# Performance work log

Measured on AMD Instinct MI355X. Metric: run time of the kernel, lower is better.

## Reference

```python
import jax, jax.numpy as jnp
import numpy as np

N_NODES = 100000
N_EDGES = 1600000
D_FEAT = 64


def setup_inputs() -> dict:
    key = jax.random.key(0)
    k1, k2, k3 = jax.random.split(key, 3)
    features = jax.random.normal(k1, (N_NODES, D_FEAT), dtype=jnp.float32)
    row = jax.random.randint(k2, (N_EDGES,), 0, N_NODES, dtype=jnp.int64 if jax.config.jax_enable_x64 else jnp.int32)
    col = jax.random.randint(k3, (N_EDGES,), 0, N_NODES, dtype=jnp.int64 if jax.config.jax_enable_x64 else jnp.int32)
    return {"features": features, "row": row, "col": col}


def reference(features, row, col):
    # adj @ H  ==  segment-sum of H[col] grouped by row (COO SpMM)
    n = features.shape[0]
    gathered = features[col]                                  # [E, d] irregular gather
    summed = jax.ops.segment_sum(gathered, row, num_segments=n)  # [N, d]
    # deg = clip(adj.sum(1), 1, None) -> per-row nonzero count
    ones = jnp.ones((row.shape[0],), dtype=features.dtype)
    deg = jax.ops.segment_sum(ones, row, num_segments=n)
    deg = jnp.clip(deg, 1.0, None)
    agg = summed / deg[:, None]
    # combine: residual add
    return features + agg
```

## Files before the change

### kernel.cpp

```cpp
#include <hip/hip_runtime.h>

#define D_FEAT 64
#define CB 256
#define CBITS 8
#define NB2MAX 512
#define E_BLK 8192
#define TMAX 256
#define SCAP 4608

__device__ inline unsigned short f2bf(float f) {
    unsigned u = __float_as_uint(f);
    u += 0x7FFFu + ((u >> 16) & 1u);
    return (unsigned short)(u >> 16);
}
__device__ inline float bf_lo(unsigned u) { return __uint_as_float(u << 16); }
__device__ inline float bf_hi(unsigned u) { return __uint_as_float(u & 0xFFFF0000u); }

__global__ __launch_bounds__(1024, 4)
void bin5_conv_kernel(const int* __restrict__ row, const int* __restrict__ col,
                      int* __restrict__ tilebuf,
                      int* __restrict__ csumG,
                      int n_edges, int ebt, int nb2,
                      const float* __restrict__ feat,
                      unsigned short* __restrict__ feat_bf, int n4) {
    int gb = blockIdx.x;
    int t = threadIdx.x;
    if (gb < ebt) {
        __shared__ int hist[NB2MAX];
        __shared__ int scn[NB2MAX];
        __shared__ int ebuf[E_BLK];
        for (int i = t; i < nb2; i += 1024) hist[i] = 0;
        __syncthreads();
        int e0 = gb * E_BLK, e1 = min(e0 + E_BLK, n_edges);
        int ne = e1 - e0;
        int rr[8], cc[8];
        #pragma unroll
        for (int k = 0; k < 8; ++k) {
            int i = t + k * 1024;
            if (i < ne) { rr[k] = row[e0 + i]; cc[k] = col[e0 + i]; }
            else rr[k] = -1;
        }
        #pragma unroll
        for (int k = 0; k < 8; ++k)
            if (rr[k] >= 0) atomicAdd(&hist[rr[k] >> CBITS], 1);
        __syncthreads();
        if (t < nb2) scn[t] = hist[t];
        __syncthreads();
        for (int o = 1; o < nb2; o <<= 1) {
            int v = (t < nb2 && t >= o) ? scn[t - o] : 0;
            __syncthreads();
            if (t < nb2) scn[t] += v;
            __syncthreads();
        }
        if (t < nb2) hist[t] = scn[t] - hist[t];
        __syncthreads();
        for (int i = t; i < nb2 + 1; i += 1024)
            csumG[(size_t)gb * (nb2 + 1) + i] = (i < nb2) ? hist[i] : ne;
        __syncthreads();
        #pragma unroll
        for (int k = 0; k < 8; ++k) {
            if (rr[k] >= 0) {
                int b = rr[k] >> CBITS;
                int pos = atomicAdd(&hist[b], 1);
                ebuf[pos] = ((rr[k] & (CB - 1)) << 17) | cc[k];
            }
        }
        __syncthreads();
        for (int i = t; i < ne; i += 1024)
            tilebuf[(size_t)gb * E_BLK + i] = ebuf[i];
    } else {
        int i = (gb - ebt) * 1024 + t;
        if (i < n4) {
            float4 f = reinterpret_cast<const float4*>(feat)[i];
            ushort4 u;
            u.x = f2bf(f.x); u.y = f2bf(f.y); u.z = f2bf(f.z); u.w = f2bf(f.w);
            reinterpret_cast<ushort4*>(feat_bf)[i] = u;
        }
    }
}

template<int BF>
__global__ __launch_bounds__(1024, 8)
void agg7_kernel(const float* __restrict__ feat,
                 const unsigned short* __restrict__ feat_bf,
                 const int* __restrict__ tilebuf,
                 const int* __restrict__ csumG,
                 float* __restrict__ out, int n_nodes, int ebt, int nb2) {
    __shared__ int tstart[TMAX], tlen[TMAX], psum[TMAX];
    __shared__ int scol[SCAP];
    __shared__ int cnt[CB], csum[CB], cur[CB], ddeg[CB];

    int cb = blockIdx.x;
    int t = threadIdx.x;
    int w = t >> 6, lane = t & 63;
    int q = lane >> 3, sub = lane & 7;
    int rA = w * 16 + q;
    int rB = rA + 8;

    for (int i = t; i < ebt; i += 1024) {
        int s = csumG[(size_t)i * (nb2 + 1) + cb];
        int e = csumG[(size_t)i * (nb2 + 1) + cb + 1];
        tstart[i] = s; tlen[i] = e - s;
    }
    if (t < CB) ddeg[t] = 0;
    __syncthreads();
    if (t < ebt) psum[t] = tlen[t];
    __syncthreads();
    for (int o = 1; o < ebt; o <<= 1) {
        int v = (t < ebt && t >= o) ? psum[t - o] : 0;
        __syncthreads();
        if (t < ebt) psum[t] += v;
        __syncthreads();
    }
    int total = psum[ebt - 1];

    float acc[16];
    #pragma unroll
    for (int k = 0; k < 16; ++k) acc[k] = 0.f;

#define GATHER(cv, o0)                                                         \
    do {                                                                       \
        if (BF) {                                                              \
            uint4 d = *reinterpret_cast<const uint4*>(                         \
                feat_bf + (size_t)(cv)*D_FEAT + sub * 8);                      \
            acc[o0+0] += bf_lo(d.x); acc[o0+1] += bf_hi(d.x);                  \
            acc[o0+2] += bf_lo(d.y); acc[o0+3] += bf_hi(d.y);                  \
            acc[o0+4] += bf_lo(d.z); acc[o0+5] += bf_hi(d.z);                  \
            acc[o0+6] += bf_lo(d.w); acc[o0+7] += bf_hi(d.w);                  \
        } else {                                                               \
            float4 x0 = *reinterpret_cast<const float4*>(                      \
                feat + (size_t)(cv)*D_FEAT + sub * 8);                         \
            float4 x1 = *reinterpret_cast<const float4*>(                      \
                feat + (size_t)(cv)*D_FEAT + sub * 8 + 4);                     \
            acc[o0+0] += x0.x; acc[o0+1] += x0.y;                              \
            acc[o0+2] += x0.z; acc[o0+3] += x0.w;                              \
            acc[o0+4] += x1.x; acc[o0+5] += x1.y;                              \
            acc[o0+6] += x1.z; acc[o0+7] += x1.w;                              \
        }                                                                      \
    } while (0)

    for (int L = 0; L < total; L += SCAP) {
        int R = min(L + SCAP, total);
        if (t < CB) cnt[t] = 0;
        __syncthreads();
        for (int tt = w; tt < ebt; tt += 16) {
            int pre = psum[tt] - tlen[tt];
            int lo = max(L - pre, 0), hi = min(tlen[tt], R - pre);
            const int* tp = tilebuf + (size_t)tt * E_BLK + tstart[tt];
            for (int i = lo + lane; i < hi; i += 64)
                atomicAdd(&cnt[((unsigned)tp[i]) >> 17], 1);
        }
        __syncthreads();
        if (t < CB) csum[t] = cnt[t];
        __syncthreads();
        for (int o = 1; o < CB; o <<= 1) {
            int v = (t < CB && t >= o) ? csum[t - o] : 0;
            __syncthreads();
            if (t < CB) csum[t] += v;
            __syncthreads();
        }
        if (t < CB) { cur[t] = csum[t] - cnt[t]; ddeg[t] += cnt[t]; }
        __syncthreads();
        for (int tt = w; tt < ebt; tt += 16) {
            int pre = psum[tt] - tlen[tt];
            int lo = max(L - pre, 0), hi = min(tlen[tt], R - pre);
            const int* tp = tilebuf + (size_t)tt * E_BLK + tstart[tt];
            for (int i = lo + lane; i < hi; i += 64) {
                int pk = tp[i];
                scol[atomicAdd(&cur[((unsigned)pk) >> 17], 1)] = pk & 0x1FFFF;
            }
        }
        __syncthreads();
        int cA = cnt[rA], sA = csum[rA] - cA;
        int cB2 = cnt[rB], sB = csum[rB] - cB2;
        int m = max(cA, cB2);
        #pragma unroll 2
        for (int j = 0; j < m; ++j) {
            if (j < cA) { int c = scol[sA + j]; GATHER(c, 0); }
            if (j < cB2) { int c = scol[sB + j]; GATHER(c, 8); }
        }
        __syncthreads();
    }
#undef GATHER

    {
        int r = cb * CB + rA;
        if (r < n_nodes) {
            float inv = 1.0f / fmaxf((float)ddeg[rA], 1.0f);
            size_t off = (size_t)r * D_FEAT + sub * 8;
            float4 f0 = *reinterpret_cast<const float4*>(feat + off);
            float4 f1 = *reinterpret_cast<const float4*>(feat + off + 4);
            float4 o0, o1;
            o0.x = f0.x + acc[0] * inv; o0.y = f0.y + acc[1] * inv;
            o0.z = f0.z + acc[2] * inv; o0.w = f0.w + acc[3] * inv;
            o1.x = f1.x + acc[4] * inv; o1.y = f1.y + acc[5] * inv;
            o1.z = f1.z + acc[6] * inv; o1.w = f1.w + acc[7] * inv;
            *reinterpret_cast<float4*>(out + off) = o0;
            *reinterpret_cast<float4*>(out + off + 4) = o1;
        }
        r = cb * CB + rB;
        if (r < n_nodes) {
            float inv = 1.0f / fmaxf((float)ddeg[rB], 1.0f);
            size_t off = (size_t)r * D_FEAT + sub * 8;
            float4 f0 = *reinterpret_cast<const float4*>(feat + off);
            float4 f1 = *reinterpret_cast<const float4*>(feat + off + 4);
            float4 o0, o1;
            o0.x = f0.x + acc[8]  * inv; o0.y = f0.y + acc[9]  * inv;
            o0.z = f0.z + acc[10] * inv; o0.w = f0.w + acc[11] * inv;
            o1.x = f1.x + acc[12] * inv; o1.y = f1.y + acc[13] * inv;
            o1.z = f1.z + acc[14] * inv; o1.w = f1.w + acc[15] * inv;
            *reinterpret_cast<float4*>(out + off) = o0;
            *reinterpret_cast<float4*>(out + off + 4) = o1;
        }
    }
}

extern "C" void kernel_launch(void* const* d_in, const int* in_sizes, int n_in,
                              void* d_out, int out_size, void* d_ws, size_t ws_size,
                              hipStream_t stream) {
    const float* feat = (const float*)d_in[0];
    const int* row = (const int*)d_in[1];
    const int* col = (const int*)d_in[2];
    float* out = (float*)d_out;

    const int n_nodes = in_sizes[0] / D_FEAT;
    const int n_edges = in_sizes[1];
    const int nb2 = (n_nodes + CB - 1) / CB;
    const int ebt = (n_edges + E_BLK - 1) / E_BLK;
    const int n4 = n_nodes * D_FEAT / 4;

    size_t tb_bytes  = (size_t)ebt * E_BLK * 4;
    size_t cs_bytes  = (size_t)ebt * (nb2 + 1) * 4;
    size_t bf_bytes  = (size_t)n_nodes * D_FEAT * 2;

    size_t lean_need = tb_bytes + cs_bytes + 256;
    size_t fat_need  = lean_need + ((bf_bytes + 63) & ~(size_t)63);
    bool fat = (ws_size >= fat_need);

    char* ws = (char*)d_ws;
    size_t p = 0;
    int* tilebuf = (int*)(ws + p); p += tb_bytes;
    int* csumG   = (int*)(ws + p); p += cs_bytes;
    p = (p + 63) & ~(size_t)63;
    unsigned short* feat_bf = nullptr;
    if (fat) { feat_bf = (unsigned short*)(ws + p); }

    {
        int conv_blocks = fat ? (n4 + 1023) / 1024 : 0;
        bin5_conv_kernel<<<ebt + conv_blocks, 1024, 0, stream>>>(
            row, col, tilebuf, csumG, n_edges, ebt, nb2,
            feat, feat_bf, fat ? n4 : 0);
    }
    if (fat) {
        agg7_kernel<1><<<nb2, 1024, 0, stream>>>(
            feat, feat_bf, tilebuf, csumG, out, n_nodes, ebt, nb2);
    } else {
        agg7_kernel<0><<<nb2, 1024, 0, stream>>>(
            feat, nullptr, tilebuf, csumG, out, n_nodes, ebt, nb2);
    }
}
```

Baseline: 134.7 us.

## Sub-sort edges by column slab and flatten tile traversal with binary search

The binning kernel now uses 512-thread blocks with 4096-edge tiles, and replaces its shared-memory Hillis-Steele scan with a wave-shuffle scan. The aggregation kernel loads each edge once into registers, finding its source tile by binary search over the prefix sums, instead of reading the tile buffer twice per chunk. It then counting-sorts edges by (row, column slab) so gathers within a slab touch a narrower range of feature rows, aiming for better L2 locality. The cost is more shared memory (bigger key arrays and a 1024-wide scan), lower occupancy (launch bounds 2 instead of 8), and eight slab passes per chunk, each ending in a barrier.

```diff
diff --git a/kernel.cpp b/kernel.cpp
--- a/kernel.cpp
+++ b/kernel.cpp
@@ -3,10 +3,14 @@
 #define D_FEAT 64
 #define CB 256
 #define CBITS 8
-#define NB2MAX 512
-#define E_BLK 8192
-#define TMAX 256
+#define NBC 448
+#define NSLAB 8
+#define SLBITS 14
+#define E_BLK 4096
+#define TMAX 512
 #define SCAP 4608
+#define KEYS (CB * NSLAB)
+#define PKN 5
 
 __device__ inline unsigned short f2bf(float f) {
     unsigned u = __float_as_uint(f);
@@ -16,8 +20,8 @@
 __device__ inline float bf_lo(unsigned u) { return __uint_as_float(u << 16); }
 __device__ inline float bf_hi(unsigned u) { return __uint_as_float(u & 0xFFFF0000u); }
 
-__global__ __launch_bounds__(1024, 4)
-void bin5_conv_kernel(const int* __restrict__ row, const int* __restrict__ col,
+__global__ __launch_bounds__(512, 4)
+void bin6_conv_kernel(const int* __restrict__ row, const int* __restrict__ col,
                       int* __restrict__ tilebuf,
                       int* __restrict__ csumG,
                       int n_edges, int ebt, int nb2,
@@ -26,17 +30,18 @@
     int gb = blockIdx.x;
     int t = threadIdx.x;
     if (gb < ebt) {
-        __shared__ int hist[NB2MAX];
-        __shared__ int scn[NB2MAX];
+        __shared__ int hist[NBC];
         __shared__ int ebuf[E_BLK];
-        for (int i = t; i < nb2; i += 1024) hist[i] = 0;
+        __shared__ int wpart[8];
+        int w = t >> 6, lane = t & 63;
+        for (int i = t; i < nb2; i += 512) hist[i] = 0;
         __syncthreads();
         int e0 = gb * E_BLK, e1 = min(e0 + E_BLK, n_edges);
         int ne = e1 - e0;
         int rr[8], cc[8];
         #pragma unroll
         for (int k = 0; k < 8; ++k) {
-            int i = t + k * 1024;
+            int i = t + k * 512;
             if (i < ne) { rr[k] = row[e0 + i]; cc[k] = col[e0 + i]; }
             else rr[k] = -1;
         }
@@ -44,18 +49,31 @@
         for (int k = 0; k < 8; ++k)
             if (rr[k] >= 0) atomicAdd(&hist[rr[k] >> CBITS], 1);
         __syncthreads();
-        if (t < nb2) scn[t] = hist[t];
-        __syncthreads();
-        for (int o = 1; o < nb2; o <<= 1) {
-            int v = (t < nb2 && t >= o) ? scn[t - o] : 0;
-            __syncthreads();
-            if (t < nb2) scn[t] += v;
-            __syncthreads();
-        }
-        if (t < nb2) hist[t] = scn[t] - hist[t];
-        __syncthreads();
-        for (int i = t; i < nb2 + 1; i += 1024)
-            csumG[(size_t)gb * (nb2 + 1) + i] = (i < nb2) ? hist[i] : ne;
+        int idx = w * 64 + lane;
+        int v = 0, incl = 0;
+        if (w < 7) {
+            v = (idx < nb2) ? hist[idx] : 0;
+            incl = v;
+            #pragma unroll
+            for (int o = 1; o < 64; o <<= 1) {
+                int up = __shfl_up(incl, o, 64);
+                if (lane >= o) incl += up;
+            }
+            if (lane == 63) wpart[w] = incl;
+        }
+        __syncthreads();
+        if (t == 0) {
+            int run = 0;
+            #pragma unroll
+            for (int k = 0; k < 7; ++k) { int x = wpart[k]; wpart[k] = run; run += x; }
+        }
+        __syncthreads();
+        if (w < 7 && idx < nb2) {
+            int excl = incl - v + wpart[w];
+            csumG[(size_t)gb * (nb2 + 1) + idx] = excl;
+            hist[idx] = excl;
+        }
+        if (t == 0) csumG[(size_t)gb * (nb2 + 1) + nb2] = ne;
         __syncthreads();
         #pragma unroll
         for (int k = 0; k < 8; ++k) {
@@ -66,10 +84,10 @@
             }
         }
         __syncthreads();
-        for (int i = t; i < ne; i += 1024)
+        for (int i = t; i < ne; i += 512)
             tilebuf[(size_t)gb * E_BLK + i] = ebuf[i];
     } else {
-        int i = (gb - ebt) * 1024 + t;
+        int i = (gb - ebt) * 512 + t;
         if (i < n4) {
             float4 f = reinterpret_cast<const float4*>(feat)[i];
             ushort4 u;
@@ -80,15 +98,18 @@
 }
 
 template<int BF>
-__global__ __launch_bounds__(1024, 8)
-void agg7_kernel(const float* __restrict__ feat,
+__global__ __launch_bounds__(1024, 2)
+void agg8_kernel(const float* __restrict__ feat,
                  const unsigned short* __restrict__ feat_bf,
                  const int* __restrict__ tilebuf,
                  const int* __restrict__ csumG,
                  float* __restrict__ out, int n_nodes, int ebt, int nb2) {
     __shared__ int tstart[TMAX], tlen[TMAX], psum[TMAX];
     __shared__ int scol[SCAP];
-    __shared__ int cnt[CB], csum[CB], cur[CB], ddeg[CB];
+    __shared__ int cnt2[KEYS], incl2[KEYS], cur2[KEYS];
+    __shared__ int ddeg[CB];
+    __shared__ int sred[1024];
+    __shared__ int wpart[8];
 
     int cb = blockIdx.x;
     int t = threadIdx.x;
@@ -104,12 +125,27 @@
     }
     if (t < CB) ddeg[t] = 0;
     __syncthreads();
-    if (t < ebt) psum[t] = tlen[t];
-    __syncthreads();
-    for (int o = 1; o < ebt; o <<= 1) {
-        int v = (t < ebt && t >= o) ? psum[t - o] : 0;
-        __syncthreads();
-        if (t < ebt) psum[t] += v;
+    {
+        int idx = w * 64 + lane;
+        int v = 0, incl = 0;
+        if (w < 7) {
+            v = (idx < ebt) ? tlen[idx] : 0;
+            incl = v;
+            #pragma unroll
+            for (int o = 1; o < 64; o <<= 1) {
+                int up = __shfl_up(incl, o, 64);
+                if (lane >= o) incl += up;
+            }
+            if (lane == 63) wpart[w] = incl;
+        }
+        __syncthreads();
+        if (t == 0) {
+            int run = 0;
+            #pragma unroll
+            for (int k = 0; k < 7; ++k) { int x = wpart[k]; wpart[k] = run; run += x; }
+        }
+        __syncthreads();
+        if (w < 7 && idx < ebt) psum[idx] = incl + wpart[w];
         __syncthreads();
     }
     int total = psum[ebt - 1];
@@ -141,45 +177,69 @@
 
     for (int L = 0; L < total; L += SCAP) {
         int R = min(L + SCAP, total);
-        if (t < CB) cnt[t] = 0;
-        __syncthreads();
-        for (int tt = w; tt < ebt; tt += 16) {
-            int pre = psum[tt] - tlen[tt];
-            int lo = max(L - pre, 0), hi = min(tlen[tt], R - pre);
-            const int* tp = tilebuf + (size_t)tt * E_BLK + tstart[tt];
-            for (int i = lo + lane; i < hi; i += 64)
-                atomicAdd(&cnt[((unsigned)tp[i]) >> 17], 1);
-        }
-        __syncthreads();
-        if (t < CB) csum[t] = cnt[t];
-        __syncthreads();
-        for (int o = 1; o < CB; o <<= 1) {
-            int v = (t < CB && t >= o) ? csum[t - o] : 0;
+        for (int i = t; i < KEYS; i += 1024) cnt2[i] = 0;
+        __syncthreads();
+        int pkr[PKN];
+        #pragma unroll
+        for (int k = 0; k < PKN; ++k) {
+            int j = L + t + k * 1024;
+            pkr[k] = -1;
+            if (j < R) {
+                int lo = 0, hi = ebt - 1;
+                #pragma unroll 9
+                while (lo < hi) { int mid = (lo + hi) >> 1;
+                                  if (psum[mid] > j) hi = mid; else lo = mid + 1; }
+                int local = j - (psum[lo] - tlen[lo]);
+                pkr[k] = tilebuf[(size_t)lo * E_BLK + tstart[lo] + local];
+            }
+        }
+        #pragma unroll
+        for (int k = 0; k < PKN; ++k) {
+            if (pkr[k] >= 0) {
+                int key = (((unsigned)pkr[k]) >> 17) * NSLAB
+                        + ((pkr[k] & 0x1FFFF) >> SLBITS);
+                atomicAdd(&cnt2[key], 1);
+            }
+        }
+        __syncthreads();
+        int a = cnt2[2 * t], bb = cnt2[2 * t + 1];
+        sred[t] = a + bb;
+        __syncthreads();
+        for (int o = 1; o < 1024; o <<= 1) {
+            int x = (t >= o) ? sred[t - o] : 0;
             __syncthreads();
-            if (t < CB) csum[t] += v;
+            sred[t] += x;
             __syncthreads();
         }
-        if (t < CB) { cur[t] = csum[t] - cnt[t]; ddeg[t] += cnt[t]; }
-        __syncthreads();
-        for (int tt = w; tt < ebt; tt += 16) {
-            int pre = psum[tt] - tlen[tt];
-            int lo = max(L - pre, 0), hi = min(tlen[tt], R - pre);
-            const int* tp = tilebuf + (size_t)tt * E_BLK + tstart[tt];
-            for (int i = lo + lane; i < hi; i += 64) {
-                int pk = tp[i];
-                scol[atomicAdd(&cur[((unsigned)pk) >> 17], 1)] = pk & 0x1FFFF;
-            }
-        }
-        __syncthreads();
-        int cA = cnt[rA], sA = csum[rA] - cA;
-        int cB2 = cnt[rB], sB = csum[rB] - cB2;
-        int m = max(cA, cB2);
-        #pragma unroll 2
-        for (int j = 0; j < m; ++j) {
-            if (j < cA) { int c = scol[sA + j]; GATHER(c, 0); }
-            if (j < cB2) { int c = scol[sB + j]; GATHER(c, 8); }
-        }
-        __syncthreads();
+        int ep = sred[t] - (a + bb);
+        incl2[2 * t] = ep + a;
+        incl2[2 * t + 1] = ep + a + bb;
+        cur2[2 * t] = ep;
+        cur2[2 * t + 1] = ep + a;
+        __syncthreads();
+        if (t < CB) ddeg[t] += incl2[t * NSLAB + NSLAB - 1]
+                             - incl2[t * NSLAB] + cnt2[t * NSLAB];
+        #pragma unroll
+        for (int k = 0; k < PKN; ++k) {
+            if (pkr[k] >= 0) {
+                int cval = pkr[k] & 0x1FFFF;
+                int key = (((unsigned)pkr[k]) >> 17) * NSLAB + (cval >> SLBITS);
+                scol[atomicAdd(&cur2[key], 1)] = cval;
+            }
+        }
+        __syncthreads();
+        for (int s = 0; s < NSLAB; ++s) {
+            int kA = rA * NSLAB + s, kB = rB * NSLAB + s;
+            int lenA = cnt2[kA], sA = incl2[kA] - lenA;
+            int lenB = cnt2[kB], sB = incl2[kB] - lenB;
+            int m = max(lenA, lenB);
+            #pragma unroll 2
+            for (int j = 0; j < m; ++j) {
+                if (j < lenA) { int c = scol[sA + j]; GATHER(c, 0); }
+                if (j < lenB) { int c = scol[sB + j]; GATHER(c, 8); }
+            }
+            __syncthreads();
+        }
     }
 #undef GATHER
 
@@ -246,16 +306,16 @@
     if (fat) { feat_bf = (unsigned short*)(ws + p); }
 
     {
-        int conv_blocks = fat ? (n4 + 1023) / 1024 : 0;
-        bin5_conv_kernel<<<ebt + conv_blocks, 1024, 0, stream>>>(
+        int conv_blocks = fat ? (n4 + 511) / 512 : 0;
+        bin6_conv_kernel<<<ebt + conv_blocks, 512, 0, stream>>>(
             row, col, tilebuf, csumG, n_edges, ebt, nb2,
             feat, feat_bf, fat ? n4 : 0);
     }
     if (fat) {
-        agg7_kernel<1><<<nb2, 1024, 0, stream>>>(
+        agg8_kernel<1><<<nb2, 1024, 0, stream>>>(
             feat, feat_bf, tilebuf, csumG, out, n_nodes, ebt, nb2);
     } else {
-        agg7_kernel<0><<<nb2, 1024, 0, stream>>>(
+        agg8_kernel<0><<<nb2, 1024, 0, stream>>>(
             feat, nullptr, tilebuf, csumG, out, n_nodes, ebt, nb2);
     }
 }
```

Result: slower. 188.8 us (+40.2%).

## Shrink row-chunks and edge tiles, load packed edges once per pass via binary search

Applied to the files above, without the earlier changes.

Halves the row-chunk size to 128 rows and the edge tile to 4096 edges, and drops blocks to 512 threads, so the aggregation grid has more, smaller blocks. In the aggregation kernel, each thread now finds its edges with a binary search over the per-tile prefix sums and keeps up to five packed edges in registers. Those edges feed both the count and the scatter phases, so tilebuf is read once per pass instead of twice. The binning kernel scans a fixed 1024-entry histogram with two elements per thread. The cost is a per-edge binary search, more partial tiles per chunk, and a larger csum table, and ebt must now fit in 512 and nb2 in 1024.

```diff
diff --git a/kernel.cpp b/kernel.cpp
--- a/kernel.cpp
+++ b/kernel.cpp
@@ -1,12 +1,13 @@
 #include <hip/hip_runtime.h>
 
 #define D_FEAT 64
-#define CB 256
-#define CBITS 8
-#define NB2MAX 512
-#define E_BLK 8192
-#define TMAX 256
-#define SCAP 4608
+#define CB 128
+#define CBITS 7
+#define NBPAD 1024
+#define E_BLK 4096
+#define EBTPAD 512
+#define SCAP 2560
+#define PKN 5
 
 __device__ inline unsigned short f2bf(float f) {
     unsigned u = __float_as_uint(f);
@@ -16,8 +17,8 @@
 __device__ inline float bf_lo(unsigned u) { return __uint_as_float(u << 16); }
 __device__ inline float bf_hi(unsigned u) { return __uint_as_float(u & 0xFFFF0000u); }
 
-__global__ __launch_bounds__(1024, 4)
-void bin5_conv_kernel(const int* __restrict__ row, const int* __restrict__ col,
+__global__ __launch_bounds__(512, 8)
+void bin7_conv_kernel(const int* __restrict__ row, const int* __restrict__ col,
                       int* __restrict__ tilebuf,
                       int* __restrict__ csumG,
                       int n_edges, int ebt, int nb2,
@@ -26,17 +27,17 @@
     int gb = blockIdx.x;
     int t = threadIdx.x;
     if (gb < ebt) {
-        __shared__ int hist[NB2MAX];
-        __shared__ int scn[NB2MAX];
+        __shared__ int hist[NBPAD];
+        __shared__ int cura[NBPAD];
         __shared__ int ebuf[E_BLK];
-        for (int i = t; i < nb2; i += 1024) hist[i] = 0;
-        __syncthreads();
-        int e0 = gb * E_BLK, e1 = min(e0 + E_BLK, n_edges);
-        int ne = e1 - e0;
+        for (int i = t; i < NBPAD; i += 512) hist[i] = 0;
+        __syncthreads();
+        int e0 = gb * E_BLK;
+        int ne = min(E_BLK, n_edges - e0);
         int rr[8], cc[8];
         #pragma unroll
         for (int k = 0; k < 8; ++k) {
-            int i = t + k * 1024;
+            int i = t + k * 512;
             if (i < ne) { rr[k] = row[e0 + i]; cc[k] = col[e0 + i]; }
             else rr[k] = -1;
         }
@@ -44,32 +45,31 @@
         for (int k = 0; k < 8; ++k)
             if (rr[k] >= 0) atomicAdd(&hist[rr[k] >> CBITS], 1);
         __syncthreads();
-        if (t < nb2) scn[t] = hist[t];
-        __syncthreads();
-        for (int o = 1; o < nb2; o <<= 1) {
-            int v = (t < nb2 && t >= o) ? scn[t - o] : 0;
-            __syncthreads();
-            if (t < nb2) scn[t] += v;
-            __syncthreads();
-        }
-        if (t < nb2) hist[t] = scn[t] - hist[t];
-        __syncthreads();
-        for (int i = t; i < nb2 + 1; i += 1024)
-            csumG[(size_t)gb * (nb2 + 1) + i] = (i < nb2) ? hist[i] : ne;
+        for (int o = 1; o < NBPAD; o <<= 1) {
+            int v0 = (t >= o) ? hist[t - o] : 0;
+            int v1 = hist[t + 512 - o];
+            __syncthreads();
+            hist[t] += v0; hist[t + 512] += v1;
+            __syncthreads();
+        }
+        cura[t] = (t == 0) ? 0 : hist[t - 1];
+        cura[t + 512] = hist[t + 511];
+        for (int i = t; i < nb2 + 1; i += 512)
+            csumG[(size_t)gb * (nb2 + 1) + i] = (i == 0) ? 0 : hist[i - 1];
         __syncthreads();
         #pragma unroll
         for (int k = 0; k < 8; ++k) {
             if (rr[k] >= 0) {
                 int b = rr[k] >> CBITS;
-                int pos = atomicAdd(&hist[b], 1);
+                int pos = atomicAdd(&cura[b], 1);
                 ebuf[pos] = ((rr[k] & (CB - 1)) << 17) | cc[k];
             }
         }
         __syncthreads();
-        for (int i = t; i < ne; i += 1024)
+        for (int i = t; i < ne; i += 512)
             tilebuf[(size_t)gb * E_BLK + i] = ebuf[i];
     } else {
-        int i = (gb - ebt) * 1024 + t;
+        int i = (gb - ebt) * 512 + t;
         if (i < n4) {
             float4 f = reinterpret_cast<const float4*>(feat)[i];
             ushort4 u;
@@ -80,36 +80,37 @@
 }
 
 template<int BF>
-__global__ __launch_bounds__(1024, 8)
-void agg7_kernel(const float* __restrict__ feat,
+__global__ __launch_bounds__(512, 8)
+void agg9_kernel(const float* __restrict__ feat,
                  const unsigned short* __restrict__ feat_bf,
                  const int* __restrict__ tilebuf,
                  const int* __restrict__ csumG,
                  float* __restrict__ out, int n_nodes, int ebt, int nb2) {
-    __shared__ int tstart[TMAX], tlen[TMAX], psum[TMAX];
+    __shared__ int tstart[EBTPAD], tlen[EBTPAD], psum[EBTPAD];
     __shared__ int scol[SCAP];
-    __shared__ int cnt[CB], csum[CB], cur[CB], ddeg[CB];
+    __shared__ int cnt[CB], incl[CB], cur[CB], ddeg[CB];
 
     int cb = blockIdx.x;
     int t = threadIdx.x;
     int w = t >> 6, lane = t & 63;
-    int q = lane >> 3, sub = lane & 7;
-    int rA = w * 16 + q;
-    int rB = rA + 8;
-
-    for (int i = t; i < ebt; i += 1024) {
+    int g = w * 8 + (lane >> 3);
+    int sub = lane & 7;
+    int rA = g;
+    int rB = g + 64;
+
+    for (int i = t; i < ebt; i += 512) {
         int s = csumG[(size_t)i * (nb2 + 1) + cb];
         int e = csumG[(size_t)i * (nb2 + 1) + cb + 1];
         tstart[i] = s; tlen[i] = e - s;
     }
     if (t < CB) ddeg[t] = 0;
     __syncthreads();
-    if (t < ebt) psum[t] = tlen[t];
+    psum[t] = (t < ebt) ? tlen[t] : 0;
     __syncthreads();
-    for (int o = 1; o < ebt; o <<= 1) {
-        int v = (t < ebt && t >= o) ? psum[t - o] : 0;
-        __syncthreads();
-        if (t < ebt) psum[t] += v;
+    for (int o = 1; o < EBTPAD; o <<= 1) {
+        int v = (t >= o) ? psum[t - o] : 0;
+        __syncthreads();
+        psum[t] += v;
         __syncthreads();
     }
     int total = psum[ebt - 1];
@@ -143,40 +144,47 @@
         int R = min(L + SCAP, total);
         if (t < CB) cnt[t] = 0;
         __syncthreads();
-        for (int tt = w; tt < ebt; tt += 16) {
-            int pre = psum[tt] - tlen[tt];
-            int lo = max(L - pre, 0), hi = min(tlen[tt], R - pre);
-            const int* tp = tilebuf + (size_t)tt * E_BLK + tstart[tt];
-            for (int i = lo + lane; i < hi; i += 64)
-                atomicAdd(&cnt[((unsigned)tp[i]) >> 17], 1);
-        }
-        __syncthreads();
-        if (t < CB) csum[t] = cnt[t];
+        int pkr[PKN];
+        #pragma unroll
+        for (int k = 0; k < PKN; ++k) {
+            int j = L + t + k * 512;
+            pkr[k] = -1;
+            if (j < R) {
+                int lo = 0, hi = ebt - 1;
+                while (lo < hi) { int mid = (lo + hi) >> 1;
+                                  if (psum[mid] > j) hi = mid; else lo = mid + 1; }
+                int local = j - (psum[lo] - tlen[lo]);
+                pkr[k] = tilebuf[(size_t)lo * E_BLK + tstart[lo] + local];
+            }
+        }
+        #pragma unroll
+        for (int k = 0; k < PKN; ++k)
+            if (pkr[k] >= 0) atomicAdd(&cnt[((unsigned)pkr[k]) >> 17], 1);
+        __syncthreads();
+        if (t < CB) incl[t] = cnt[t];
         __syncthreads();
         for (int o = 1; o < CB; o <<= 1) {
-            int v = (t < CB && t >= o) ? csum[t - o] : 0;
-            __syncthreads();
-            if (t < CB) csum[t] += v;
-            __syncthreads();
-        }
-        if (t < CB) { cur[t] = csum[t] - cnt[t]; ddeg[t] += cnt[t]; }
-        __syncthreads();
-        for (int tt = w; tt < ebt; tt += 16) {
-            int pre = psum[tt] - tlen[tt];
-            int lo = max(L - pre, 0), hi = min(tlen[tt], R - pre);
-            const int* tp = tilebuf + (size_t)tt * E_BLK + tstart[tt];
-            for (int i = lo + lane; i < hi; i += 64) {
-                int pk = tp[i];
-                scol[atomicAdd(&cur[((unsigned)pk) >> 17], 1)] = pk & 0x1FFFF;
+            int v = (t < CB && t >= o) ? incl[t - o] : 0;
+            __syncthreads();
+            if (t < CB) incl[t] += v;
+            __syncthreads();
+        }
+        if (t < CB) { cur[t] = incl[t] - cnt[t]; ddeg[t] += cnt[t]; }
+        __syncthreads();
+        #pragma unroll
+        for (int k = 0; k < PKN; ++k) {
+            if (pkr[k] >= 0) {
+                int key = ((unsigned)pkr[k]) >> 17;
+                scol[atomicAdd(&cur[key], 1)] = pkr[k] & 0x1FFFF;
             }
         }
         __syncthreads();
-        int cA = cnt[rA], sA = csum[rA] - cA;
-        int cB2 = cnt[rB], sB = csum[rB] - cB2;
+        int cA = cnt[rA], sA = incl[rA] - cA;
+        int cB2 = cnt[rB], sB = incl[rB] - cB2;
         int m = max(cA, cB2);
         #pragma unroll 2
         for (int j = 0; j < m; ++j) {
-            if (j < cA) { int c = scol[sA + j]; GATHER(c, 0); }
+            if (j < cA)  { int c = scol[sA + j]; GATHER(c, 0); }
             if (j < cB2) { int c = scol[sB + j]; GATHER(c, 8); }
         }
         __syncthreads();
@@ -246,16 +254,16 @@
     if (fat) { feat_bf = (unsigned short*)(ws + p); }
 
     {
-        int conv_blocks = fat ? (n4 + 1023) / 1024 : 0;
-        bin5_conv_kernel<<<ebt + conv_blocks, 1024, 0, stream>>>(
+        int conv_blocks = fat ? (n4 + 511) / 512 : 0;
+        bin7_conv_kernel<<<ebt + conv_blocks, 512, 0, stream>>>(
             row, col, tilebuf, csumG, n_edges, ebt, nb2,
             feat, feat_bf, fat ? n4 : 0);
     }
     if (fat) {
-        agg7_kernel<1><<<nb2, 1024, 0, stream>>>(
+        agg9_kernel<1><<<nb2, 512, 0, stream>>>(
             feat, feat_bf, tilebuf, csumG, out, n_nodes, ebt, nb2);
     } else {
-        agg7_kernel<0><<<nb2, 1024, 0, stream>>>(
+        agg9_kernel<0><<<nb2, 512, 0, stream>>>(
             feat, nullptr, tilebuf, csumG, out, n_nodes, ebt, nb2);
     }
 }
```

Result: slower. 148.7 us (+10.4%).
